# Performance work log

Hardware: AMD Instinct MI355X
Metric: run time of the kernel (lower is better)

## Reference

```python
import jax, jax.numpy as jnp
import numpy as np

QMIN = 0.0
QMAX = 255.0  # uint8, asymmetric


def fake_quant(x, scale, zp):
    # asymmetric uint8 fake-quantization: q = clamp(round(x/s + zp), 0, 255); dq = (q - zp) * s
    s = scale.reshape(())
    z = zp.reshape(())
    q = jnp.clip(jnp.round(x / s + z), QMIN, QMAX)
    return (q - z) * s


def setup_inputs() -> dict:
    key = jax.random.key(0)
    k1, k2 = jax.random.split(key)
    B, M, K, N = 4, 2048, 4096, 4096
    x1 = jax.random.normal(k1, (B, M, K), dtype=jnp.float32)
    x2 = jax.random.normal(k2, (B, K, N), dtype=jnp.float32)
    # realistic learned per-tensor scale / zero-point for ~N(0,1) data over uint8 range
    x1_scale = jnp.full((1,), 8.0 / 255.0, dtype=jnp.float32)
    x1_zp = jnp.full((1,), 128.0, dtype=jnp.float32)
    x2_scale = jnp.full((1,), 8.0 / 255.0, dtype=jnp.float32)
    x2_zp = jnp.full((1,), 128.0, dtype=jnp.float32)
    return {"x1": x1, "x2": x2, "x1_scale": x1_scale, "x1_zp": x1_zp,
            "x2_scale": x2_scale, "x2_zp": x2_zp}


def reference(x1, x2, x1_scale, x1_zp, x2_scale, x2_zp):
    q1 = fake_quant(x1, x1_scale, x1_zp)  # [B, M, K]
    q2 = fake_quant(x2, x2_scale, x2_zp)  # [B, K, N]
    return jnp.matmul(q1, q2)             # [B, M, N]
```

## Files before the change

kernel.cpp:

```cpp
#include <hip/hip_runtime.h>
#include <stdint.h>

typedef int v4i __attribute__((ext_vector_type(4)));

#define GLOBAL_AS __attribute__((address_space(1)))
#define LDS_AS __attribute__((address_space(3)))

__device__ __forceinline__ int quant1(float x, float s, float z, int zi) {
    float q = rintf(x / s + z);
    q = fminf(fmaxf(q, 0.0f), 255.0f);
    return (int)q - zi;
}

__device__ __forceinline__ unsigned qpack4(float4 v, float s, float z, int zi) {
    unsigned q0 = (unsigned)(quant1(v.x, s, z, zi) & 255);
    unsigned q1 = (unsigned)(quant1(v.y, s, z, zi) & 255);
    unsigned q2 = (unsigned)(quant1(v.z, s, z, zi) & 255);
    unsigned q3 = (unsigned)(quant1(v.w, s, z, zi) & 255);
    return q0 | (q1 << 8) | (q2 << 16) | (q3 << 24);
}

__global__ __launch_bounds__(256) void quant_lin(const float* __restrict__ x,
                                                 int8_t* __restrict__ out,
                                                 const float* __restrict__ sp,
                                                 const float* __restrict__ zp,
                                                 long n16) {
    float s = sp[0], z = zp[0];
    int zi = (int)rintf(z);
    long i = (long)blockIdx.x * 256 + threadIdx.x;
    if (i >= n16) return;
    const float4* xv = (const float4*)x;
    uint4 w;
    w.x = qpack4(xv[i * 4 + 0], s, z, zi);
    w.y = qpack4(xv[i * 4 + 1], s, z, zi);
    w.z = qpack4(xv[i * 4 + 2], s, z, zi);
    w.w = qpack4(xv[i * 4 + 3], s, z, zi);
    ((uint4*)out)[i] = w;
}

__global__ __launch_bounds__(256) void quant_bt(const float* __restrict__ x,
                                                int8_t* __restrict__ out,
                                                const float* __restrict__ sp,
                                                const float* __restrict__ zp) {
    constexpr int K = 4096, N = 4096;
    float s = sp[0], z = zp[0];
    int zi = (int)rintf(z);
    size_t bin = (size_t)blockIdx.z * K * N;
    int tid = threadIdx.x;
    int bk = tid >> 4;
    int bn = tid & 15;
    int k0 = blockIdx.y * 64, n0 = blockIdx.x * 64;
    __shared__ unsigned lds[64][17];
    unsigned o0 = 0, o1 = 0, o2 = 0, o3 = 0;
#pragma unroll
    for (int r = 0; r < 4; ++r) {
        float4 v = *(const float4*)(x + bin + (size_t)(k0 + bk * 4 + r) * N + n0 + bn * 4);
        o0 |= (unsigned)(quant1(v.x, s, z, zi) & 255) << (r * 8);
        o1 |= (unsigned)(quant1(v.y, s, z, zi) & 255) << (r * 8);
        o2 |= (unsigned)(quant1(v.z, s, z, zi) & 255) << (r * 8);
        o3 |= (unsigned)(quant1(v.w, s, z, zi) & 255) << (r * 8);
    }
    lds[bn * 4 + 0][bk] = o0;
    lds[bn * 4 + 1][bk] = o1;
    lds[bn * 4 + 2][bk] = o2;
    lds[bn * 4 + 3][bk] = o3;
    __syncthreads();
    int nl = tid >> 2, ch = tid & 3;
    uint4 w;
    w.x = lds[nl][ch * 4 + 0];
    w.y = lds[nl][ch * 4 + 1];
    w.z = lds[nl][ch * 4 + 2];
    w.w = lds[nl][ch * 4 + 3];
    *(uint4*)(out + bin + (size_t)(n0 + nl) * K + k0 + ch * 16) = w;
}

__global__ __launch_bounds__(512, 2) void gemm_i8(const int8_t* __restrict__ A,
                                                  const int8_t* __restrict__ Bt,
                                                  float* __restrict__ C,
                                                  const float* __restrict__ sp1,
                                                  const float* __restrict__ sp2) {
    constexpr int M = 2048, N = 4096, K = 4096;
    constexpr int BM = 256, BN = 256, BK = 128;
    constexpr int NT = K / BK;
    constexpr int NBN = N / BN;

    extern __shared__ char smem[];

    int b = blockIdx.z;
    const int8_t* Ab = A + (size_t)b * M * K;
    const int8_t* Bb = Bt + (size_t)b * N * K;
    float* Cb = C + (size_t)b * M * N;

    int nwg = gridDim.x;
    int wg = blockIdx.x;
    wg = (wg & 7) * (nwg >> 3) + (wg >> 3);
    int by = wg / NBN, bx = wg % NBN;
    int m0 = by * BM, n0 = bx * BN;

    int tid = threadIdx.x;
    int lane = tid & 63, wid = tid >> 6;
    int wr = wid >> 2, wc = wid & 3;
    int l15 = lane & 15, cb = lane >> 4;

    const int8_t* Abase = Ab + (size_t)m0 * K;
    const int8_t* Bbase = Bb + (size_t)n0 * K;

    int aoff[8], boff[4];
#pragma unroll
    for (int m = 0; m < 8; ++m) {
        int r = wr * 128 + m * 16 + l15;
        aoff[m] = r * 64 + ((cb ^ ((r >> 1) & 3)) * 16);
    }
#pragma unroll
    for (int n = 0; n < 4; ++n) {
        int r = wc * 64 + n * 16 + l15;
        boff[n] = r * 64 + ((cb ^ ((r >> 1) & 3)) * 16);
    }

    v4i zero = {0, 0, 0, 0};
    v4i acc[8][4];
#pragma unroll
    for (int m = 0; m < 8; ++m)
#pragma unroll
        for (int n = 0; n < 4; ++n) acc[m][n] = zero;

#define ISSUE(mat, base, jt1, kh)                                                      \
    {                                                                                  \
        const int8_t* gb = (base) + (size_t)(jt1) * BK + (size_t)(kh) * 64;            \
        char* dst = smem + ((((jt1) & 1) * 2 + (mat)) * 2 + (kh)) * 16384;             \
        _Pragma("unroll") for (int j = 0; j < 2; ++j) {                                \
            int idx = j * 512 + tid;                                                   \
            int row = idx >> 2;                                                        \
            int cc = idx & 3;                                                          \
            int sc_ = cc ^ ((row >> 1) & 3);                                           \
            __builtin_amdgcn_global_load_lds(                                          \
                (const GLOBAL_AS void*)(gb + (size_t)row * K + sc_ * 16),              \
                (LDS_AS void*)(dst + idx * 16), 16, 0, 0);                             \
        }                                                                              \
    }

#define PHASE(buf, kk, mh, DOISSUE, DOWAIT)                                            \
    {                                                                                  \
        const char* Ar = smem + ((buf) * 4 + 0 + (kk)) * 16384;                        \
        const char* Br = smem + ((buf) * 4 + 2 + (kk)) * 16384;                        \
        v4i af[4], bf[4];                                                              \
        _Pragma("unroll") for (int m = 0; m < 4; ++m)                                  \
            af[m] = *(const v4i*)(Ar + aoff[(mh) * 4 + m]);                            \
        _Pragma("unroll") for (int n = 0; n < 4; ++n)                                  \
            bf[n] = *(const v4i*)(Br + boff[n]);                                       \
        DOISSUE;                                                                       \
        __builtin_amdgcn_s_barrier();                                                  \
        asm volatile("s_waitcnt lgkmcnt(0)" ::: "memory");                             \
        __builtin_amdgcn_sched_barrier(0);                                             \
        __builtin_amdgcn_s_setprio(1);                                                 \
        _Pragma("unroll") for (int m = 0; m < 4; ++m)                                  \
            _Pragma("unroll") for (int n = 0; n < 4; ++n)                              \
                acc[(mh) * 4 + m][n] = __builtin_amdgcn_mfma_i32_16x16x64_i8(          \
                    af[m], bf[n], acc[(mh) * 4 + m][n], 0, 0, 0);                      \
        __builtin_amdgcn_s_setprio(0);                                                 \
        DOWAIT;                                                                        \
        __builtin_amdgcn_s_barrier();                                                  \
    }

    ISSUE(0, Abase, 0, 0);
    ISSUE(1, Bbase, 0, 0);
    ISSUE(0, Abase, 0, 1);
    ISSUE(1, Bbase, 0, 1);
    asm volatile("s_waitcnt vmcnt(4)" ::: "memory");
    __builtin_amdgcn_s_barrier();

    for (int jt = 0; jt < NT; ++jt) {
        int buf = jt & 1;
        if (jt + 1 < NT) {
            PHASE(buf, 0, 0, ISSUE(0, Abase, jt + 1, 0), )
            PHASE(buf, 0, 1, ISSUE(1, Bbase, jt + 1, 0),
                  asm volatile("s_waitcnt vmcnt(4)" ::: "memory"))
            PHASE(buf, 1, 0, ISSUE(0, Abase, jt + 1, 1), )
            PHASE(buf, 1, 1, ISSUE(1, Bbase, jt + 1, 1),
                  asm volatile("s_waitcnt vmcnt(4)" ::: "memory"))
        } else {
            PHASE(buf, 0, 0, , )
            PHASE(buf, 0, 1, , asm volatile("s_waitcnt vmcnt(0)" ::: "memory"))
            PHASE(buf, 1, 0, , )
            PHASE(buf, 1, 1, , )
        }
    }

    float sc = sp1[0] * sp2[0];
    int r0 = cb * 4;
#pragma unroll
    for (int m = 0; m < 8; ++m) {
#pragma unroll
        for (int n = 0; n < 4; ++n) {
            float* p = Cb + (size_t)(m0 + wr * 128 + m * 16 + r0) * N +
                       (n0 + wc * 64 + n * 16 + l15);
#pragma unroll
            for (int r = 0; r < 4; ++r) p[(size_t)r * N] = sc * (float)acc[m][n][r];
        }
    }
#undef ISSUE
#undef PHASE
}

extern "C" void kernel_launch(void* const* d_in, const int* in_sizes, int n_in,
                              void* d_out, int out_size, void* d_ws, size_t ws_size,
                              hipStream_t stream) {
    const float* x1 = (const float*)d_in[0];
    const float* x2 = (const float*)d_in[1];
    const float* s1 = (const float*)d_in[2];
    const float* z1 = (const float*)d_in[3];
    const float* s2 = (const float*)d_in[4];
    const float* z2 = (const float*)d_in[5];
    float* out = (float*)d_out;

    const int B = 4, M = 2048, K = 4096, N = 4096;
    const size_t ASZ = (size_t)B * M * K;
    const size_t BSZ = (size_t)B * K * N;
    dim3 blk(256);

    static int lds_attr_set = 0;
    if (!lds_attr_set) {
        (void)hipFuncSetAttribute((const void*)gemm_i8,
                                  hipFuncAttributeMaxDynamicSharedMemorySize, 131072);
        lds_attr_set = 1;
    }

    if (ws_size >= ASZ + BSZ) {
        int8_t* Aq = (int8_t*)d_ws;
        int8_t* Bq = Aq + ASZ;
        long n16 = (long)(ASZ / 16);
        quant_lin<<<dim3((unsigned)(n16 / 256)), blk, 0, stream>>>(x1, Aq, s1, z1, n16);
        quant_bt<<<dim3(N / 64, K / 64, B), blk, 0, stream>>>(x2, Bq, s2, z2);
        gemm_i8<<<dim3((M / 256) * (N / 256), 1, B), dim3(512), 131072, stream>>>(
            Aq, Bq, out, s1, s2);
    } else {
        const size_t AB = (size_t)M * K, BB = (size_t)K * N;
        int8_t* Aq = (int8_t*)d_ws;
        int8_t* Bq = Aq + AB;
        for (int b = 0; b < B; ++b) {
            long n16 = (long)(AB / 16);
            quant_lin<<<dim3((unsigned)(n16 / 256)), blk, 0, stream>>>(x1 + (size_t)b * AB, Aq, s1, z1, n16);
            quant_bt<<<dim3(N / 64, K / 64, 1), blk, 0, stream>>>(x2 + (size_t)b * BB, Bq, s2, z2);
            gemm_i8<<<dim3((M / 256) * (N / 256), 1, 1), dim3(512), 131072, stream>>>(
                Aq, Bq, out + (size_t)b * M * N, s1, s2);
        }
    }
}
```

Baseline: 260.5 us.

## Replace per-phase barriers with one sync per K-tile and precomputed load pointers

The int8 MFMA main loop drops its four-phase structure, which had two s_barriers and explicit vmcnt/lgkmcnt waits per phase. It now uses a single __syncthreads per K tile, relying on compiler-inserted waits. Global-to-LDS load addresses become incrementing pointers computed once, instead of recomputing row and swizzle math on every issue, and the B fragment is reused across both M halves rather than reloaded. This cuts synchronization and address overhead, but the loads of the next tile may now sit in less tightly scheduled waits, and the overlap between loads and MFMA is left to the compiler.

Measured after the change: 262.8 us. No clear change (+0.9%).

```diff
diff --git a/kernel.cpp b/kernel.cpp
--- a/kernel.cpp
+++ b/kernel.cpp
@@ -105,6 +105,15 @@
     const int8_t* Abase = Ab + (size_t)m0 * K;
     const int8_t* Bbase = Bb + (size_t)n0 * K;
 
+    int row0 = tid >> 2, cc0 = tid & 3;
+    int sw0 = cc0 ^ ((row0 >> 1) & 3);
+    const size_t JSTEP = (size_t)128 * K;
+    const int8_t* pA0 = Abase + (size_t)row0 * K + sw0 * 16;
+    const int8_t* pA1 = pA0 + 64;
+    const int8_t* pB0 = Bbase + (size_t)row0 * K + sw0 * 16;
+    const int8_t* pB1 = pB0 + 64;
+    const unsigned dbase = (unsigned)tid * 16;
+
     int aoff[8], boff[4];
 #pragma unroll
     for (int m = 0; m < 8; ++m) {
@@ -124,66 +133,64 @@
 #pragma unroll
         for (int n = 0; n < 4; ++n) acc[m][n] = zero;
 
-#define ISSUE(mat, base, jt1, kh)                                                      \
+#define ISSUE(p, mat, kh, buf)                                                         \
     {                                                                                  \
-        const int8_t* gb = (base) + (size_t)(jt1) * BK + (size_t)(kh) * 64;            \
-        char* dst = smem + ((((jt1) & 1) * 2 + (mat)) * 2 + (kh)) * 16384;             \
-        _Pragma("unroll") for (int j = 0; j < 2; ++j) {                                \
-            int idx = j * 512 + tid;                                                   \
-            int row = idx >> 2;                                                        \
-            int cc = idx & 3;                                                          \
-            int sc_ = cc ^ ((row >> 1) & 3);                                           \
-            __builtin_amdgcn_global_load_lds(                                          \
-                (const GLOBAL_AS void*)(gb + (size_t)row * K + sc_ * 16),              \
-                (LDS_AS void*)(dst + idx * 16), 16, 0, 0);                             \
-        }                                                                              \
-    }
-
-#define PHASE(buf, kk, mh, DOISSUE, DOWAIT)                                            \
+        char* dst = smem + ((((buf)*2 + (mat)) * 2 + (kh)) * 16384) + dbase;           \
+        __builtin_amdgcn_global_load_lds((const GLOBAL_AS void*)(p),                   \
+                                         (LDS_AS void*)dst, 16, 0, 0);                 \
+        __builtin_amdgcn_global_load_lds((const GLOBAL_AS void*)((p) + JSTEP),         \
+                                         (LDS_AS void*)(dst + 8192), 16, 0, 0);        \
+    }
+
+#define LDA(Ar, h)                                                                     \
+    _Pragma("unroll") for (int m = 0; m < 4; ++m)                                      \
+        af[m] = *(const v4i*)((Ar) + aoff[(h)*4 + m]);
+
+#define LDB(Br)                                                                        \
+    _Pragma("unroll") for (int n = 0; n < 4; ++n)                                      \
+        bf[n] = *(const v4i*)((Br) + boff[n]);
+
+#define MM(mh)                                                                         \
     {                                                                                  \
-        const char* Ar = smem + ((buf) * 4 + 0 + (kk)) * 16384;                        \
-        const char* Br = smem + ((buf) * 4 + 2 + (kk)) * 16384;                        \
-        v4i af[4], bf[4];                                                              \
-        _Pragma("unroll") for (int m = 0; m < 4; ++m)                                  \
-            af[m] = *(const v4i*)(Ar + aoff[(mh) * 4 + m]);                            \
-        _Pragma("unroll") for (int n = 0; n < 4; ++n)                                  \
-            bf[n] = *(const v4i*)(Br + boff[n]);                                       \
-        DOISSUE;                                                                       \
-        __builtin_amdgcn_s_barrier();                                                  \
-        asm volatile("s_waitcnt lgkmcnt(0)" ::: "memory");                             \
-        __builtin_amdgcn_sched_barrier(0);                                             \
         __builtin_amdgcn_s_setprio(1);                                                 \
         _Pragma("unroll") for (int m = 0; m < 4; ++m)                                  \
             _Pragma("unroll") for (int n = 0; n < 4; ++n)                              \
-                acc[(mh) * 4 + m][n] = __builtin_amdgcn_mfma_i32_16x16x64_i8(          \
-                    af[m], bf[n], acc[(mh) * 4 + m][n], 0, 0, 0);                      \
+                acc[(mh)*4 + m][n] = __builtin_amdgcn_mfma_i32_16x16x64_i8(            \
+                    af[m], bf[n], acc[(mh)*4 + m][n], 0, 0, 0);                        \
         __builtin_amdgcn_s_setprio(0);                                                 \
-        DOWAIT;                                                                        \
-        __builtin_amdgcn_s_barrier();                                                  \
-    }
-
-    ISSUE(0, Abase, 0, 0);
-    ISSUE(1, Bbase, 0, 0);
-    ISSUE(0, Abase, 0, 1);
-    ISSUE(1, Bbase, 0, 1);
-    asm volatile("s_waitcnt vmcnt(4)" ::: "memory");
-    __builtin_amdgcn_s_barrier();
+    }
+
+    ISSUE(pA0, 0, 0, 0);
+    ISSUE(pB0, 1, 0, 0);
+    ISSUE(pA1, 0, 1, 0);
+    ISSUE(pB1, 1, 1, 0);
+    __syncthreads();
 
     for (int jt = 0; jt < NT; ++jt) {
         int buf = jt & 1;
-        if (jt + 1 < NT) {
-            PHASE(buf, 0, 0, ISSUE(0, Abase, jt + 1, 0), )
-            PHASE(buf, 0, 1, ISSUE(1, Bbase, jt + 1, 0),
-                  asm volatile("s_waitcnt vmcnt(4)" ::: "memory"))
-            PHASE(buf, 1, 0, ISSUE(0, Abase, jt + 1, 1), )
-            PHASE(buf, 1, 1, ISSUE(1, Bbase, jt + 1, 1),
-                  asm volatile("s_waitcnt vmcnt(4)" ::: "memory"))
-        } else {
-            PHASE(buf, 0, 0, , )
-            PHASE(buf, 0, 1, , asm volatile("s_waitcnt vmcnt(0)" ::: "memory"))
-            PHASE(buf, 1, 0, , )
-            PHASE(buf, 1, 1, , )
-        }
+        const char* Ar0 = smem + (buf * 4 + 0) * 16384;
+        const char* Ar1 = smem + (buf * 4 + 1) * 16384;
+        const char* Br0 = smem + (buf * 4 + 2) * 16384;
+        const char* Br1 = smem + (buf * 4 + 3) * 16384;
+        bool pf = (jt + 1 < NT);
+        pA0 += BK; pA1 += BK; pB0 += BK; pB1 += BK;
+
+        v4i af[4], bf[4];
+        LDB(Br0);
+        LDA(Ar0, 0);
+        if (pf) ISSUE(pA0, 0, 0, buf ^ 1);
+        MM(0);
+        LDA(Ar0, 1);
+        if (pf) ISSUE(pB0, 1, 0, buf ^ 1);
+        MM(1);
+        LDB(Br1);
+        LDA(Ar1, 0);
+        if (pf) ISSUE(pA1, 0, 1, buf ^ 1);
+        MM(0);
+        LDA(Ar1, 1);
+        if (pf) ISSUE(pB1, 1, 1, buf ^ 1);
+        MM(1);
+        __syncthreads();
     }
 
     float sc = sp1[0] * sp2[0];
@@ -199,7 +206,9 @@
         }
     }
 #undef ISSUE
-#undef PHASE
+#undef LDA
+#undef LDB
+#undef MM
 }
 
 extern "C" void kernel_launch(void* const* d_in, const int* in_sizes, int n_in,
```
